# Kernel tuning notes

Hardware: AMD Instinct MI355X
Metric: run time of the kernel (lower is better)

## Reference

```python
import jax, jax.numpy as jnp
import numpy as np

TOTAL_NODES = 262144
NUM_GRAPHS = 1024
MAX_NODES = 512
D = 256


def setup_inputs() -> dict:
    key = jax.random.key(0)
    k1, k2 = jax.random.split(key)
    node_emb = jax.random.normal(k1, (TOTAL_NODES, D), dtype=jnp.float32)
    batch_idx = jnp.sort(jax.random.randint(k2, (TOTAL_NODES,), 0, NUM_GRAPHS, dtype=jnp.int64))
    return {"node_emb": node_emb, "batch_idx": batch_idx,
            "num_graphs": NUM_GRAPHS, "max_nodes": MAX_NODES}


def reference(node_emb, batch_idx, num_graphs, max_nodes):
    # counts[g] = number of nodes in graph g  (torch.bincount)
    n = node_emb.shape[0]
    counts = jax.ops.segment_sum(jnp.ones((n,), dtype=jnp.int32), batch_idx,
                                 num_segments=num_graphs)
    # exclusive prefix sum -> start offset of each graph's node block
    starts = jnp.cumsum(counts) - counts
    # position of each node within its graph (batch_idx is sorted)
    pos = jnp.arange(n, dtype=jnp.int32) - starts[batch_idx]
    # single fused scatter replacing the per-graph python loop
    enc_states = jnp.zeros((num_graphs, max_nodes, node_emb.shape[-1]),
                           dtype=node_emb.dtype)
    enc_states = enc_states.at[batch_idx, pos].set(node_emb)
    # mask: first counts[g] slots of each row are 1
    enc_mask = (jnp.arange(max_nodes, dtype=jnp.int32)[None, :]
                < counts[:, None]).astype(jnp.int32)
    return enc_states, enc_mask
```

## Files before the change

### kernel.cpp

```cpp
#include <hip/hip_runtime.h>

#define NUM_GRAPHS 1024
#define MAX_NODES  512
#define DIM        256
#define D4         (DIM / 4)

typedef float f4 __attribute__((ext_vector_type(4)));

__global__ void scan_offsets_kernel(const int* __restrict__ bidx32, int n,
                                    int* __restrict__ starts) {
    int i = blockIdx.x * blockDim.x + threadIdx.x;
    if (i >= n) return;
    const bool is64 = (bidx32[n - 1] == 0);
    const int cur  = is64 ? bidx32[2 * i] : bidx32[i];
    const int prev = (i == 0) ? -1 : (is64 ? bidx32[2 * (i - 1)] : bidx32[i - 1]);
    for (int g = prev + 1; g <= cur; ++g) starts[g] = i;
    if (i == n - 1) {
        for (int g = cur + 1; g <= NUM_GRAPHS; ++g) starts[g] = n;
    }
}

__global__ void __launch_bounds__(256)
scatter_states_kernel(const f4* __restrict__ emb,
                      const int* __restrict__ starts,
                      f4* __restrict__ out,
                      float* __restrict__ mask) {
    const int b    = blockIdx.x;
    const int g    = b >> 1;
    const int half = b & 1;
    const int s    = starts[g];
    const int c    = starts[g + 1] - s;
    const int lane = threadIdx.x & 63;
    const int wid  = threadIdx.x >> 6;
    const int slot0 = half * 256 + wid;

    f4* outb = out + (size_t)(g * MAX_NODES + half * 256) * D4;

#pragma unroll 8
    for (int it = 0; it < 64; ++it) {
        const int slot = slot0 + it * 4;
        f4 val = (f4)(0.f);
        if (slot < c) {
            val = __builtin_nontemporal_load(&emb[(size_t)(s + slot) * D4 + lane]);
        }
        __builtin_nontemporal_store(val, &outb[it * 256 + threadIdx.x]);
    }

    const int mslot = half * 256 + threadIdx.x;
    __builtin_nontemporal_store((mslot < c) ? 1.0f : 0.0f,
                                &mask[g * MAX_NODES + mslot]);
}

extern "C" void kernel_launch(void* const* d_in, const int* in_sizes, int n_in,
                              void* d_out, int out_size, void* d_ws, size_t ws_size,
                              hipStream_t stream) {
    const float* node_emb = (const float*)d_in[0];
    const int*   bidx32   = (const int*)d_in[1];
    const int    n        = in_sizes[1];

    int* starts = (int*)d_ws;

    scan_offsets_kernel<<<(n + 255) / 256, 256, 0, stream>>>(bidx32, n, starts);

    float* mask = (float*)d_out + (size_t)NUM_GRAPHS * MAX_NODES * DIM;
    scatter_states_kernel<<<NUM_GRAPHS * 2, 256, 0, stream>>>(
        (const f4*)node_emb, starts, (f4*)d_out, mask);
}
```

Measured before the change: 189.6 us.

## Fuse offset computation into scatter via per-block binary search

Removes the separate scan kernel and its launch. Each block instead finds its graph's start and end with two binary searches over the sorted batch index, done by two threads and shared through LDS. The copy loop is also reorganised so each wave handles a contiguous 64-row chunk, splitting the real copy from the zero fill so no per-row branch is needed. Nontemporal loads and stores are replaced with ordinary ones. This adds a serial ~18-step dependent-load search at the start of every block and changes the cache behaviour of the large streaming write.

```diff
diff --git a/kernel.cpp b/kernel.cpp
--- a/kernel.cpp
+++ b/kernel.cpp
@@ -7,48 +7,55 @@
 
 typedef float f4 __attribute__((ext_vector_type(4)));
 
-__global__ void scan_offsets_kernel(const int* __restrict__ bidx32, int n,
-                                    int* __restrict__ starts) {
-    int i = blockIdx.x * blockDim.x + threadIdx.x;
-    if (i >= n) return;
-    const bool is64 = (bidx32[n - 1] == 0);
-    const int cur  = is64 ? bidx32[2 * i] : bidx32[i];
-    const int prev = (i == 0) ? -1 : (is64 ? bidx32[2 * (i - 1)] : bidx32[i - 1]);
-    for (int g = prev + 1; g <= cur; ++g) starts[g] = i;
-    if (i == n - 1) {
-        for (int g = cur + 1; g <= NUM_GRAPHS; ++g) starts[g] = n;
+__device__ __forceinline__ int lower_bound_idx(const int* __restrict__ b, int n,
+                                               bool is64, int key) {
+    int lo = 0, hi = n;
+    while (lo < hi) {
+        int mid = (lo + hi) >> 1;
+        int v = is64 ? b[2 * mid] : b[mid];
+        if (v < key) lo = mid + 1; else hi = mid;
     }
+    return lo;
 }
 
 __global__ void __launch_bounds__(256)
 scatter_states_kernel(const f4* __restrict__ emb,
-                      const int* __restrict__ starts,
-                      f4* __restrict__ out,
-                      float* __restrict__ mask) {
+                      const int* __restrict__ bidx32, int n,
+                      f4* __restrict__ out, float* __restrict__ mask) {
+    __shared__ int sc[2];
     const int b    = blockIdx.x;
     const int g    = b >> 1;
     const int half = b & 1;
-    const int s    = starts[g];
-    const int c    = starts[g + 1] - s;
-    const int lane = threadIdx.x & 63;
-    const int wid  = threadIdx.x >> 6;
-    const int slot0 = half * 256 + wid;
 
-    f4* outb = out + (size_t)(g * MAX_NODES + half * 256) * D4;
+    if (threadIdx.x < 2) {
+        const bool is64 = (bidx32[n - 1] == 0);
+        sc[threadIdx.x] = lower_bound_idx(bidx32, n, is64, g + threadIdx.x);
+    }
+    __syncthreads();
+    const int s = sc[0];
+    const int c = sc[1] - sc[0];
 
+    const int lane  = threadIdx.x & 63;
+    const int w     = threadIdx.x >> 6;
+    const int rbase = half * 256 + w * 64;
+
+    const f4* wemb = emb + (size_t)(s + rbase) * D4 + lane;
+    f4*       wout = out + ((size_t)g * MAX_NODES + rbase) * D4 + lane;
+
+    int ncopy = c - rbase;
+    ncopy = ncopy < 0 ? 0 : (ncopy > 64 ? 64 : ncopy);
+
+    int it = 0;
 #pragma unroll 8
-    for (int it = 0; it < 64; ++it) {
-        const int slot = slot0 + it * 4;
-        f4 val = (f4)(0.f);
-        if (slot < c) {
-            val = __builtin_nontemporal_load(&emb[(size_t)(s + slot) * D4 + lane]);
-        }
-        __builtin_nontemporal_store(val, &outb[it * 256 + threadIdx.x]);
-    }
+    for (; it < ncopy; ++it)
+        wout[it * D4] = wemb[it * D4];
+    const f4 z = (f4)(0.f);
+#pragma unroll 8
+    for (; it < 64; ++it)
+        wout[it * D4] = z;
 
     const int mslot = half * 256 + threadIdx.x;
-    __builtin_nontemporal_store((mslot < c) ? 1.0f : 0.0f,
-                                &mask[g * MAX_NODES + mslot]);
+    mask[(size_t)g * MAX_NODES + mslot] = (mslot < c) ? 1.0f : 0.0f;
 }
 
 extern "C" void kernel_launch(void* const* d_in, const int* in_sizes, int n_in,
@@ -58,11 +65,7 @@
     const int*   bidx32   = (const int*)d_in[1];
     const int    n        = in_sizes[1];
 
-    int* starts = (int*)d_ws;
-
-    scan_offsets_kernel<<<(n + 255) / 256, 256, 0, stream>>>(bidx32, n, starts);
-
     float* mask = (float*)d_out + (size_t)NUM_GRAPHS * MAX_NODES * DIM;
     scatter_states_kernel<<<NUM_GRAPHS * 2, 256, 0, stream>>>(
-        (const f4*)node_emb, starts, (f4*)d_out, mask);
+        (const f4*)node_emb, bidx32, n, (f4*)d_out, mask);
 }
```

Measured after the change: 172.9 us, median of 2. 8.8% less time.
